# Performance work log

Measured on AMD Instinct MI355X. Metric: run time of the kernel, lower is better.

## Reference

```python
import jax, jax.numpy as jnp
import numpy as np

N_HEADS = 8
EPS = 1e-12  # F.normalize eps


def setup_inputs() -> dict:
    key = jax.random.key(0)
    ks = jax.random.split(key, 7)
    B, M, S, D = 2, 4, 2048, 512
    scale = 1.0 / np.sqrt(D)
    return {
        "x": jax.random.normal(ks[0], (B, M, S, D), dtype=jnp.float32),
        "Wq": jax.random.normal(ks[1], (D, D), dtype=jnp.float32) * scale,
        "bq": jax.random.normal(ks[2], (D,), dtype=jnp.float32) * 0.01,
        "Wkv": jax.random.normal(ks[3], (D, D), dtype=jnp.float32) * scale,
        "bkv": jax.random.normal(ks[4], (D,), dtype=jnp.float32) * 0.01,
        "Wo": jax.random.normal(ks[5], (D, D), dtype=jnp.float32) * scale,
        "bo": jax.random.normal(ks[6], (D,), dtype=jnp.float32) * 0.01,
    }


def _heads(t, H):
    # [B,M,S,D] -> [B,M,H,S,dk]
    B, Mo, S, D = t.shape
    return t.reshape(B, Mo, S, H, D // H).swapaxes(2, 3)


def reference(x, Wq, bq, Wkv, bkv, Wo, bo):
    B, Mo, S, D = x.shape
    H = N_HEADS
    # nn.Linear: y = x @ W^T + b
    Q = x @ Wq.T + bq
    KV = x @ Wkv.T + bkv  # K and V share this projection
    Qh = _heads(Q, H)
    Kh = _heads(KV, H)
    Vh = Kh
    # L2-normalize along head dim (cosine attention)
    Qn = Qh / jnp.maximum(jnp.linalg.norm(Qh, axis=-1, keepdims=True), EPS)
    Kn = Kh / jnp.maximum(jnp.linalg.norm(Kh, axis=-1, keepdims=True), EPS)
    scores = jnp.einsum("bmhqd,bmhkd->bmhqk", Qn, Kn)
    attn = jax.nn.softmax(scores, axis=-1)  # dropout=0 (eval)
    ctx = jnp.einsum("bmhqk,bmhkd->bmhqd", attn, Vh)
    ctx = ctx.swapaxes(2, 3).reshape(B, Mo, S, D)
    return ctx @ Wo.T + bo
```

## Files before the change

### kernel.cpp

```cpp
#include <hip/hip_runtime.h>

typedef __attribute__((ext_vector_type(8))) short bf16x8;
typedef __attribute__((ext_vector_type(8))) _Float16 f16x8;
typedef __attribute__((ext_vector_type(2))) _Float16 f16x2;
typedef __attribute__((ext_vector_type(4))) float f32x4;

__device__ __forceinline__ unsigned short f2bf(float f) {
  union { float f; unsigned int i; } v;
  v.f = f;
  unsigned int r = v.i + 0x7FFFu + ((v.i >> 16) & 1u);
  return (unsigned short)(r >> 16);
}

__device__ __forceinline__ f16x2 cvt_pk(float a, float b) {
  return __builtin_bit_cast(f16x2, __builtin_amdgcn_cvt_pkrtz(a, b));
}

__device__ __forceinline__ f16x2 exp_poly(f16x2 x) {
  const f16x2 a5 = {(_Float16)0.00868682f, (_Float16)0.00868682f};
  const f16x2 a4 = {(_Float16)0.04379392f, (_Float16)0.04379392f};
  const f16x2 a3 = {(_Float16)0.16648887f, (_Float16)0.16648887f};
  const f16x2 a2 = {(_Float16)0.49919676f, (_Float16)0.49919676f};
  const f16x2 a1 = {(_Float16)1.00002229f, (_Float16)1.00002229f};
  const f16x2 a0 = {(_Float16)1.00004478f, (_Float16)1.00004478f};
#if __has_builtin(__builtin_elementwise_fma)
  f16x2 r = a5;
  r = __builtin_elementwise_fma(r, x, a4);
  r = __builtin_elementwise_fma(r, x, a3);
  r = __builtin_elementwise_fma(r, x, a2);
  r = __builtin_elementwise_fma(r, x, a1);
  r = __builtin_elementwise_fma(r, x, a0);
#else
  f16x2 r = a5;
  r = r * x + a4;
  r = r * x + a3;
  r = r * x + a2;
  r = r * x + a1;
  r = r * x + a0;
#endif
  return r;
}

__device__ __forceinline__ float dot2acc(f16x2 a, float acc) {
#if __has_builtin(__builtin_amdgcn_fdot2)
  const f16x2 one2 = {(_Float16)1.0f, (_Float16)1.0f};
  return __builtin_amdgcn_fdot2(a, one2, acc, false);
#else
  return acc + (float)a.x + (float)a.y;
#endif
}

__global__ __launch_bounds__(256) void cvt_all(
    const float* __restrict__ x, const float* __restrict__ wq,
    const float* __restrict__ wkv, const float* __restrict__ wo,
    unsigned short* __restrict__ xb, unsigned short* __restrict__ wqb,
    unsigned short* __restrict__ wkvb, unsigned short* __restrict__ wob) {
  int b = blockIdx.x;
  const float* in;
  unsigned short* out;
  int i;
  if (b < 8192) { in = x; out = xb; i = b * 256 + threadIdx.x; }
  else if (b < 8448) { in = wq; out = wqb; i = (b - 8192) * 256 + threadIdx.x; }
  else if (b < 8704) { in = wkv; out = wkvb; i = (b - 8448) * 256 + threadIdx.x; }
  else { in = wo; out = wob; i = (b - 8704) * 256 + threadIdx.x; }
  float4 v = ((const float4*)in)[i];
  ushort4 o;
  o.x = f2bf(v.x);
  o.y = f2bf(v.y);
  o.z = f2bf(v.z);
  o.w = f2bf(v.w);
  ((ushort4*)out)[i] = o;
}

__global__ __launch_bounds__(256) void gemm_qkv(
    const unsigned short* __restrict__ A, const unsigned short* __restrict__ Wq,
    const unsigned short* __restrict__ Wkv, const float* __restrict__ bq,
    const float* __restrict__ bkv, unsigned short* __restrict__ Qn,
    unsigned short* __restrict__ Vt, unsigned short* __restrict__ Kn) {
  __shared__ unsigned short lA[128 * 72];
  __shared__ unsigned short lB[128 * 72];
  const int isKV = (int)(blockIdx.y >> 2);
  const unsigned short* Bt = isKV ? Wkv : Wq;
  const float* bias = isKV ? bkv : bq;
  const int tid = threadIdx.x;
  const int lane = tid & 63;
  const int quad = lane >> 4, m16 = lane & 15;
  const int w = tid >> 6;
  const int wm = w >> 1, wn = w & 1;
  const long mb = (long)blockIdx.x * 128;
  const long nb = (long)(blockIdx.y & 3) * 128;
  f32x4 acc[4][4];
#pragma unroll
  for (int i = 0; i < 4; i++)
#pragma unroll
    for (int j = 0; j < 4; j++) acc[i][j] = (f32x4){0.f, 0.f, 0.f, 0.f};

  for (int kb = 0; kb < 512; kb += 64) {
    __syncthreads();
#pragma unroll
    for (int c = tid; c < 1024; c += 256) {
      int row = c >> 3, k8 = (c & 7) << 3;
      *(uint4*)&lA[row * 72 + k8] = *(const uint4*)(A + (mb + row) * 512 + kb + k8);
      *(uint4*)&lB[row * 72 + k8] = *(const uint4*)(Bt + (nb + row) * 512 + kb + k8);
    }
    __syncthreads();
#pragma unroll
    for (int ks = 0; ks < 64; ks += 32) {
      int kq = ks + quad * 8;
      bf16x8 af[4], bfr[4];
#pragma unroll
      for (int i = 0; i < 4; i++)
        af[i] = *(const bf16x8*)&lA[(wm * 64 + i * 16 + m16) * 72 + kq];
#pragma unroll
      for (int j = 0; j < 4; j++)
        bfr[j] = *(const bf16x8*)&lB[(wn * 64 + j * 16 + m16) * 72 + kq];
#pragma unroll
      for (int i = 0; i < 4; i++)
#pragma unroll
        for (int j = 0; j < 4; j++)
          acc[i][j] =
              __builtin_amdgcn_mfma_f32_16x16x32_bf16(af[i], bfr[j], acc[i][j], 0, 0, 0);
    }
  }
#pragma unroll
  for (int i = 0; i < 4; i++) {
    long row0 = mb + wm * 64 + i * 16 + quad * 4;
    float bb[4], val[4][4], inv[4];
#pragma unroll
    for (int j = 0; j < 4; j++) {
      bb[j] = bias[nb + wn * 64 + j * 16 + m16];
#pragma unroll
      for (int r = 0; r < 4; r++) val[j][r] = acc[i][j][r] + bb[j];
    }
#pragma unroll
    for (int r = 0; r < 4; r++) {
      float s = val[0][r] * val[0][r] + val[1][r] * val[1][r] +
                val[2][r] * val[2][r] + val[3][r] * val[3][r];
      s += __shfl_xor(s, 1);
      s += __shfl_xor(s, 2);
      s += __shfl_xor(s, 4);
      s += __shfl_xor(s, 8);
      inv[r] = 1.0f / fmaxf(sqrtf(s), 1e-12f);
    }
    if (!isKV) {
#pragma unroll
      for (int r = 0; r < 4; r++)
#pragma unroll
        for (int j = 0; j < 4; j++) {
          long col = nb + wn * 64 + j * 16 + m16;
          Qn[(row0 + r) * 512 + col] = f2bf(val[j][r] * inv[r]);
        }
    } else {
#pragma unroll
      for (int r = 0; r < 4; r++)
#pragma unroll
        for (int j = 0; j < 4; j++) {
          long col = nb + wn * 64 + j * 16 + m16;
          Kn[(row0 + r) * 512 + col] = f2bf(val[j][r] * inv[r]);
        }
      int bm = (int)(row0 >> 11);
      int s0 = (int)(row0 & 2047);
#pragma unroll
      for (int j = 0; j < 4; j++) {
        int col = (int)(nb) + wn * 64 + j * 16 + m16;
        int h = col >> 6, d = col & 63;
        f16x2 lo = cvt_pk(val[j][0], val[j][1]);
        f16x2 hi = cvt_pk(val[j][2], val[j][3]);
        uint2 pk = make_uint2(__builtin_bit_cast(unsigned int, lo),
                              __builtin_bit_cast(unsigned int, hi));
        *(uint2*)(Vt + ((long)(bm * 8 + h) * 64 + d) * 2048 + s0) = pk;
      }
    }
  }
}

__global__ __launch_bounds__(256) void gemm_o(
    const unsigned short* __restrict__ A, const unsigned short* __restrict__ Bt,
    const float* __restrict__ bias, float* __restrict__ Cout) {
  __shared__ unsigned short lA[128 * 72];
  __shared__ unsigned short lB[128 * 72];
  const int tid = threadIdx.x;
  const int lane = tid & 63;
  const int quad = lane >> 4, m16 = lane & 15;
  const int w = tid >> 6;
  const int wm = w >> 1, wn = w & 1;
  const long mb = (long)blockIdx.x * 128;
  const long nb = (long)blockIdx.y * 128;
  f32x4 acc[4][4];
#pragma unroll
  for (int i = 0; i < 4; i++)
#pragma unroll
    for (int j = 0; j < 4; j++) acc[i][j] = (f32x4){0.f, 0.f, 0.f, 0.f};

  for (int kb = 0; kb < 512; kb += 64) {
    __syncthreads();
#pragma unroll
    for (int c = tid; c < 1024; c += 256) {
      int row = c >> 3, k8 = (c & 7) << 3;
      *(uint4*)&lA[row * 72 + k8] = *(const uint4*)(A + (mb + row) * 512 + kb + k8);
      *(uint4*)&lB[row * 72 + k8] = *(const uint4*)(Bt + (nb + row) * 512 + kb + k8);
    }
    __syncthreads();
#pragma unroll
    for (int ks = 0; ks < 64; ks += 32) {
      int kq = ks + quad * 8;
      bf16x8 af[4], bfr[4];
#pragma unroll
      for (int i = 0; i < 4; i++)
        af[i] = *(const bf16x8*)&lA[(wm * 64 + i * 16 + m16) * 72 + kq];
#pragma unroll
      for (int j = 0; j < 4; j++)
        bfr[j] = *(const bf16x8*)&lB[(wn * 64 + j * 16 + m16) * 72 + kq];
#pragma unroll
      for (int i = 0; i < 4; i++)
#pragma unroll
        for (int j = 0; j < 4; j++)
          acc[i][j] =
              __builtin_amdgcn_mfma_f32_16x16x32_bf16(af[i], bfr[j], acc[i][j], 0, 0, 0);
    }
  }
#pragma unroll
  for (int i = 0; i < 4; i++) {
    long row0 = mb + wm * 64 + i * 16 + quad * 4;
#pragma unroll
    for (int j = 0; j < 4; j++) {
      long col = nb + wn * 64 + j * 16 + m16;
      float bb = bias[col];
#pragma unroll
      for (int r = 0; r < 4; r++) Cout[(row0 + r) * 512 + col] = acc[i][j][r] + bb;
    }
  }
}

__global__ __launch_bounds__(256, 4) void attn_cos(
    const unsigned short* __restrict__ Qn, const unsigned short* __restrict__ Kn,
    const unsigned short* __restrict__ Vt, unsigned short* __restrict__ ctx) {
  __shared__ unsigned short lK[64 * 72];
  __shared__ unsigned short lVt[64 * 72];
  __shared__ unsigned short lP[128 * 72];
  const int qt = blockIdx.x;
  const int g = blockIdx.y;
  const int bm = g >> 3, h = g & 7;
  const int tid = threadIdx.x;
  const int lane = tid & 63;
  const int quad = lane >> 4, m16 = lane & 15;
  const int w = tid >> 6;
  const long rowbase = (long)bm * 2048;
  const int colbase = h * 64;
  const long qrow0 = rowbase + qt * 128 + w * 32;
  const unsigned short* Kbase = Kn + rowbase * 512 + colbase;
  const unsigned short* Vbase = Vt + (long)g * 64 * 2048;

  bf16x8 qf[2][2];
#pragma unroll
  for (int i = 0; i < 2; i++)
#pragma unroll
    for (int ks = 0; ks < 2; ks++)
      qf[i][ks] = *(const bf16x8*)(Qn + (qrow0 + i * 16 + m16) * 512 + colbase +
                                   ks * 32 + quad * 8);

  f32x4 cacc[2][4];
#pragma unroll
  for (int i = 0; i < 2; i++)
#pragma unroll
    for (int j = 0; j < 4; j++) cacc[i][j] = (f32x4){0.f, 0.f, 0.f, 0.f};
  float li[2] = {0.f, 0.f};

  for (int kt = 0; kt < 32; ++kt) {
    __syncthreads();
#pragma unroll
    for (int p = 0; p < 2; ++p) {
      int c = tid + p * 256;
      int row = c >> 3, e8 = (c & 7) << 3;
      *(uint4*)&lK[row * 72 + e8] = *(const uint4*)(Kbase + (kt * 64 + row) * 512 + e8);
      *(uint4*)&lVt[row * 72 + e8] = *(const uint4*)(Vbase + row * 2048 + kt * 64 + e8);
    }
    __syncthreads();

    f32x4 sacc[4][2];
#pragma unroll
    for (int j = 0; j < 4; j++)
#pragma unroll
      for (int i = 0; i < 2; i++) sacc[j][i] = (f32x4){0.f, 0.f, 0.f, 0.f};
#pragma unroll
    for (int ks = 0; ks < 2; ++ks) {
      int dq = ks * 32 + quad * 8;
      bf16x8 kf[4];
#pragma unroll
      for (int j = 0; j < 4; j++)
        kf[j] = *(const bf16x8*)&lK[(j * 16 + m16) * 72 + dq];
#pragma unroll
      for (int j = 0; j < 4; j++)
#pragma unroll
        for (int i = 0; i < 2; i++)
          sacc[j][i] =
              __builtin_amdgcn_mfma_f32_16x16x32_bf16(kf[j], qf[i][ks], sacc[j][i], 0, 0, 0);
    }

#pragma unroll
    for (int j = 0; j < 4; j++)
#pragma unroll
      for (int i = 0; i < 2; i++) {
        f16x2 x01 = cvt_pk(sacc[j][i][0], sacc[j][i][1]);
        f16x2 x23 = cvt_pk(sacc[j][i][2], sacc[j][i][3]);
        f16x2 e01 = exp_poly(x01);
        f16x2 e23 = exp_poly(x23);
        li[i] = dot2acc(e01, li[i]);
        li[i] = dot2acc(e23, li[i]);
        uint2 pk = make_uint2(__builtin_bit_cast(unsigned int, e01),
                              __builtin_bit_cast(unsigned int, e23));
        *(uint2*)&lP[(w * 32 + i * 16 + m16) * 72 + j * 16 + quad * 4] = pk;
      }

#pragma unroll
    for (int ks = 0; ks < 2; ++ks) {
      int kq = ks * 32 + quad * 8;
      f16x8 pf[2], vf[4];
#pragma unroll
      for (int i = 0; i < 2; i++)
        pf[i] = *(const f16x8*)&lP[(w * 32 + i * 16 + m16) * 72 + kq];
#pragma unroll
      for (int j = 0; j < 4; j++)
        vf[j] = *(const f16x8*)&lVt[(j * 16 + m16) * 72 + kq];
#pragma unroll
      for (int i = 0; i < 2; i++)
#pragma unroll
        for (int j = 0; j < 4; j++)
          cacc[i][j] =
              __builtin_amdgcn_mfma_f32_16x16x32_f16(pf[i], vf[j], cacc[i][j], 0, 0, 0);
    }
  }

#pragma unroll
  for (int i = 0; i < 2; i++) {
    li[i] += __shfl_xor(li[i], 16);
    li[i] += __shfl_xor(li[i], 32);
  }
  float linv[2][4];
#pragma unroll
  for (int i = 0; i < 2; i++)
#pragma unroll
    for (int r = 0; r < 4; r++) linv[i][r] = 1.0f / __shfl(li[i], quad * 4 + r);
#pragma unroll
  for (int i = 0; i < 2; i++)
#pragma unroll
    for (int j = 0; j < 4; j++) {
      long dcol = colbase + j * 16 + m16;
#pragma unroll
      for (int r = 0; r < 4; r++) {
        long qrow = qrow0 + i * 16 + quad * 4 + r;
        ctx[qrow * 512 + dcol] = f2bf(cacc[i][j][r] * linv[i][r]);
      }
    }
}

extern "C" void kernel_launch(void* const* d_in, const int* in_sizes, int n_in,
                              void* d_out, int out_size, void* d_ws, size_t ws_size,
                              hipStream_t stream) {
  (void)in_sizes; (void)n_in; (void)out_size; (void)ws_size;
  const float* x = (const float*)d_in[0];
  const float* Wq = (const float*)d_in[1];
  const float* bq = (const float*)d_in[2];
  const float* Wkv = (const float*)d_in[3];
  const float* bkv = (const float*)d_in[4];
  const float* Wo = (const float*)d_in[5];
  const float* bo = (const float*)d_in[6];

  char* ws = (char*)d_ws;
  unsigned short* x_bf   = (unsigned short*)(ws);
  unsigned short* Wq_bf  = (unsigned short*)(ws + 16777216);
  unsigned short* Wkv_bf = (unsigned short*)(ws + 17301504);
  unsigned short* Wo_bf  = (unsigned short*)(ws + 17825792);
  unsigned short* Qn_bf  = (unsigned short*)(ws + 18350080);
  unsigned short* Kn_bf  = (unsigned short*)(ws + 35127296);
  unsigned short* Vt_f16 = (unsigned short*)(ws + 51904512);
  unsigned short* ctx_bf = x_bf;

  cvt_all<<<8960, 256, 0, stream>>>(x, Wq, Wkv, Wo, x_bf, Wq_bf, Wkv_bf, Wo_bf);

  gemm_qkv<<<dim3(128, 8), 256, 0, stream>>>(x_bf, Wq_bf, Wkv_bf, bq, bkv, Qn_bf,
                                             Vt_f16, Kn_bf);

  attn_cos<<<dim3(16, 64), 256, 0, stream>>>(Qn_bf, Kn_bf, Vt_f16, ctx_bf);

  gemm_o<<<dim3(128, 4), 256, 0, stream>>>(ctx_bf, Wo_bf, bo, (float*)d_out);
}
```

Before: 252.0 us.

## Load GEMM and attention tiles directly into LDS in MFMA fragment layout

Replaces the register-staged global-to-LDS tile copies in the QKV GEMM, output GEMM and attention kernel with global_load_lds direct transfers. Tiles are stored in a fragment-major layout so each lane reads its MFMA operand contiguously at lane*8. This removes the VGPR round trip and the padding. The P buffer switches to an XOR swizzle instead of padding, and the smaller LDS footprint lets attention raise its occupancy hint to 5 blocks. The risk is that the direct-to-LDS path and the new layouts depend on exact lane-to-address mapping, and they cost some load coalescing.

```diff
diff --git a/kernel.cpp b/kernel.cpp
--- a/kernel.cpp
+++ b/kernel.cpp
@@ -14,6 +14,12 @@
 
 __device__ __forceinline__ f16x2 cvt_pk(float a, float b) {
   return __builtin_bit_cast(f16x2, __builtin_amdgcn_cvt_pkrtz(a, b));
+}
+
+__device__ __forceinline__ void gl_lds16(const unsigned short* g, unsigned short* l) {
+  __builtin_amdgcn_global_load_lds(
+      (const __attribute__((address_space(1))) unsigned int*)g,
+      (__attribute__((address_space(3))) unsigned int*)l, 16, 0, 0);
 }
 
 __device__ __forceinline__ f16x2 exp_poly(f16x2 x) {
@@ -77,8 +83,8 @@
     const unsigned short* __restrict__ Wkv, const float* __restrict__ bq,
     const float* __restrict__ bkv, unsigned short* __restrict__ Qn,
     unsigned short* __restrict__ Vt, unsigned short* __restrict__ Kn) {
-  __shared__ unsigned short lA[128 * 72];
-  __shared__ unsigned short lB[128 * 72];
+  __shared__ __attribute__((aligned(16))) unsigned short lA[16 * 512];
+  __shared__ __attribute__((aligned(16))) unsigned short lB[16 * 512];
   const int isKV = (int)(blockIdx.y >> 2);
   const unsigned short* Bt = isKV ? Wkv : Wq;
   const float* bias = isKV ? bkv : bq;
@@ -97,23 +103,28 @@
 
   for (int kb = 0; kb < 512; kb += 64) {
     __syncthreads();
-#pragma unroll
-    for (int c = tid; c < 1024; c += 256) {
-      int row = c >> 3, k8 = (c & 7) << 3;
-      *(uint4*)&lA[row * 72 + k8] = *(const uint4*)(A + (mb + row) * 512 + kb + k8);
-      *(uint4*)&lB[row * 72 + k8] = *(const uint4*)(Bt + (nb + row) * 512 + kb + k8);
-    }
-    __syncthreads();
-#pragma unroll
-    for (int ks = 0; ks < 64; ks += 32) {
-      int kq = ks + quad * 8;
+    {
+      const unsigned short* gA = A + (mb + (2 * w) * 16 + m16) * 512 + kb + quad * 8;
+      gl_lds16(gA, &lA[(4 * w + 0) * 512]);
+      gl_lds16(gA + 32, &lA[(4 * w + 1) * 512]);
+      gl_lds16(gA + 16 * 512, &lA[(4 * w + 2) * 512]);
+      gl_lds16(gA + 16 * 512 + 32, &lA[(4 * w + 3) * 512]);
+      const unsigned short* gB = Bt + (nb + (2 * w) * 16 + m16) * 512 + kb + quad * 8;
+      gl_lds16(gB, &lB[(4 * w + 0) * 512]);
+      gl_lds16(gB + 32, &lB[(4 * w + 1) * 512]);
+      gl_lds16(gB + 16 * 512, &lB[(4 * w + 2) * 512]);
+      gl_lds16(gB + 16 * 512 + 32, &lB[(4 * w + 3) * 512]);
+    }
+    __syncthreads();
+#pragma unroll
+    for (int ks = 0; ks < 2; ks++) {
       bf16x8 af[4], bfr[4];
 #pragma unroll
       for (int i = 0; i < 4; i++)
-        af[i] = *(const bf16x8*)&lA[(wm * 64 + i * 16 + m16) * 72 + kq];
+        af[i] = *(const bf16x8*)&lA[(((wm * 4 + i) << 1) | ks) * 512 + lane * 8];
 #pragma unroll
       for (int j = 0; j < 4; j++)
-        bfr[j] = *(const bf16x8*)&lB[(wn * 64 + j * 16 + m16) * 72 + kq];
+        bfr[j] = *(const bf16x8*)&lB[(((wn * 4 + j) << 1) | ks) * 512 + lane * 8];
 #pragma unroll
       for (int i = 0; i < 4; i++)
 #pragma unroll
@@ -177,8 +188,8 @@
 __global__ __launch_bounds__(256) void gemm_o(
     const unsigned short* __restrict__ A, const unsigned short* __restrict__ Bt,
     const float* __restrict__ bias, float* __restrict__ Cout) {
-  __shared__ unsigned short lA[128 * 72];
-  __shared__ unsigned short lB[128 * 72];
+  __shared__ __attribute__((aligned(16))) unsigned short lA[16 * 512];
+  __shared__ __attribute__((aligned(16))) unsigned short lB[16 * 512];
   const int tid = threadIdx.x;
   const int lane = tid & 63;
   const int quad = lane >> 4, m16 = lane & 15;
@@ -194,23 +205,28 @@
 
   for (int kb = 0; kb < 512; kb += 64) {
     __syncthreads();
-#pragma unroll
-    for (int c = tid; c < 1024; c += 256) {
-      int row = c >> 3, k8 = (c & 7) << 3;
-      *(uint4*)&lA[row * 72 + k8] = *(const uint4*)(A + (mb + row) * 512 + kb + k8);
-      *(uint4*)&lB[row * 72 + k8] = *(const uint4*)(Bt + (nb + row) * 512 + kb + k8);
-    }
-    __syncthreads();
-#pragma unroll
-    for (int ks = 0; ks < 64; ks += 32) {
-      int kq = ks + quad * 8;
+    {
+      const unsigned short* gA = A + (mb + (2 * w) * 16 + m16) * 512 + kb + quad * 8;
+      gl_lds16(gA, &lA[(4 * w + 0) * 512]);
+      gl_lds16(gA + 32, &lA[(4 * w + 1) * 512]);
+      gl_lds16(gA + 16 * 512, &lA[(4 * w + 2) * 512]);
+      gl_lds16(gA + 16 * 512 + 32, &lA[(4 * w + 3) * 512]);
+      const unsigned short* gB = Bt + (nb + (2 * w) * 16 + m16) * 512 + kb + quad * 8;
+      gl_lds16(gB, &lB[(4 * w + 0) * 512]);
+      gl_lds16(gB + 32, &lB[(4 * w + 1) * 512]);
+      gl_lds16(gB + 16 * 512, &lB[(4 * w + 2) * 512]);
+      gl_lds16(gB + 16 * 512 + 32, &lB[(4 * w + 3) * 512]);
+    }
+    __syncthreads();
+#pragma unroll
+    for (int ks = 0; ks < 2; ks++) {
       bf16x8 af[4], bfr[4];
 #pragma unroll
       for (int i = 0; i < 4; i++)
-        af[i] = *(const bf16x8*)&lA[(wm * 64 + i * 16 + m16) * 72 + kq];
+        af[i] = *(const bf16x8*)&lA[(((wm * 4 + i) << 1) | ks) * 512 + lane * 8];
 #pragma unroll
       for (int j = 0; j < 4; j++)
-        bfr[j] = *(const bf16x8*)&lB[(wn * 64 + j * 16 + m16) * 72 + kq];
+        bfr[j] = *(const bf16x8*)&lB[(((wn * 4 + j) << 1) | ks) * 512 + lane * 8];
 #pragma unroll
       for (int i = 0; i < 4; i++)
 #pragma unroll
@@ -232,12 +248,12 @@
   }
 }
 
-__global__ __launch_bounds__(256, 4) void attn_cos(
+__global__ __launch_bounds__(256, 5) void attn_cos(
     const unsigned short* __restrict__ Qn, const unsigned short* __restrict__ Kn,
     const unsigned short* __restrict__ Vt, unsigned short* __restrict__ ctx) {
-  __shared__ unsigned short lK[64 * 72];
-  __shared__ unsigned short lVt[64 * 72];
-  __shared__ unsigned short lP[128 * 72];
+  __shared__ __attribute__((aligned(16))) unsigned short lK[8 * 512];
+  __shared__ __attribute__((aligned(16))) unsigned short lVt[8 * 512];
+  __shared__ __attribute__((aligned(16))) unsigned short lP[128 * 64];
   const int qt = blockIdx.x;
   const int g = blockIdx.y;
   const int bm = g >> 3, h = g & 7;
@@ -250,6 +266,7 @@
   const long qrow0 = rowbase + qt * 128 + w * 32;
   const unsigned short* Kbase = Kn + rowbase * 512 + colbase;
   const unsigned short* Vbase = Vt + (long)g * 64 * 2048;
+  const int swz = (m16 & 7) << 3;
 
   bf16x8 qf[2][2];
 #pragma unroll
@@ -268,12 +285,13 @@
 
   for (int kt = 0; kt < 32; ++kt) {
     __syncthreads();
-#pragma unroll
-    for (int p = 0; p < 2; ++p) {
-      int c = tid + p * 256;
-      int row = c >> 3, e8 = (c & 7) << 3;
-      *(uint4*)&lK[row * 72 + e8] = *(const uint4*)(Kbase + (kt * 64 + row) * 512 + e8);
-      *(uint4*)&lVt[row * 72 + e8] = *(const uint4*)(Vbase + row * 2048 + kt * 64 + e8);
+    {
+      const unsigned short* gK = Kbase + (kt * 64 + w * 16 + m16) * 512 + quad * 8;
+      gl_lds16(gK, &lK[(2 * w + 0) * 512]);
+      gl_lds16(gK + 32, &lK[(2 * w + 1) * 512]);
+      const unsigned short* gV = Vbase + (w * 16 + m16) * 2048 + kt * 64 + quad * 8;
+      gl_lds16(gV, &lVt[(2 * w + 0) * 512]);
+      gl_lds16(gV + 32, &lVt[(2 * w + 1) * 512]);
     }
     __syncthreads();
 
@@ -284,11 +302,10 @@
       for (int i = 0; i < 2; i++) sacc[j][i] = (f32x4){0.f, 0.f, 0.f, 0.f};
 #pragma unroll
     for (int ks = 0; ks < 2; ++ks) {
-      int dq = ks * 32 + quad * 8;
       bf16x8 kf[4];
 #pragma unroll
       for (int j = 0; j < 4; j++)
-        kf[j] = *(const bf16x8*)&lK[(j * 16 + m16) * 72 + dq];
+        kf[j] = *(const bf16x8*)&lK[((j << 1) | ks) * 512 + lane * 8];
 #pragma unroll
       for (int j = 0; j < 4; j++)
 #pragma unroll
@@ -309,19 +326,19 @@
         li[i] = dot2acc(e23, li[i]);
         uint2 pk = make_uint2(__builtin_bit_cast(unsigned int, e01),
                               __builtin_bit_cast(unsigned int, e23));
-        *(uint2*)&lP[(w * 32 + i * 16 + m16) * 72 + j * 16 + quad * 4] = pk;
+        *(uint2*)&lP[(w * 32 + i * 16 + m16) * 64 + ((j * 16 + quad * 4) ^ swz)] = pk;
       }
 
 #pragma unroll
     for (int ks = 0; ks < 2; ++ks) {
-      int kq = ks * 32 + quad * 8;
       f16x8 pf[2], vf[4];
 #pragma unroll
       for (int i = 0; i < 2; i++)
-        pf[i] = *(const f16x8*)&lP[(w * 32 + i * 16 + m16) * 72 + kq];
+        pf[i] = *(const f16x8*)&lP[(w * 32 + i * 16 + m16) * 64 +
+                                   ((ks * 32 + quad * 8) ^ swz)];
 #pragma unroll
       for (int j = 0; j < 4; j++)
-        vf[j] = *(const f16x8*)&lVt[(j * 16 + m16) * 72 + kq];
+        vf[j] = *(const f16x8*)&lVt[((j << 1) | ks) * 512 + lane * 8];
 #pragma unroll
       for (int i = 0; i < 2; i++)
 #pragma unroll
```

After: 276.7 us. 1.1x slower.
